# Performance work log

Hardware: AMD Instinct MI355X
Metric: run time of the kernel (lower is better)

Reference implementation:

```python
import jax, jax.numpy as jnp
import numpy as np

HEADS = 16

def setup_inputs() -> dict:
    key = jax.random.key(0)
    k1, k2, k3 = jax.random.split(key, 3)
    B, S, D = 2, 2048, 1024
    return {
        "query": jax.random.normal(k1, (B, S, D), dtype=jnp.float32),
        "key": jax.random.normal(k2, (B, S, D), dtype=jnp.float32),
        "value": jax.random.normal(k3, (B, S, D), dtype=jnp.float32),
    }

def reference(query, key, value):
    B, S, D = query.shape
    H = HEADS
    dh = D // H
    # split(-1) into H equal chunks == reshape to (B, S, H, dh)
    q = query.reshape(B, S, H, dh)
    k = key.reshape(B, S, H, dh)
    v = value.reshape(B, S, H, dh)
    scale = 1.0 / jnp.sqrt(jnp.asarray(dh, dtype=query.dtype))
    scores = jnp.einsum('bqhd,bkhd->bhqk', q, k) * scale  # [B,H,S,S]
    probs = jax.nn.softmax(scores, axis=-1)
    out = jnp.einsum('bhqk,bkhd->bqhd', probs, v)  # [B,S,H,dh]
    return out.reshape(B, S, D)
```

## Files before the change

### kernel.cpp

```cpp
#include <hip/hip_runtime.h>


#define B_ 2
#define S_ 2048
#define D_ 1024
#define H_ 16
#define DH 64
#define M_TILE 128
#define N_TILE 128
#define NITER (S_ / N_TILE)

typedef __bf16 bf16;
typedef __bf16 bf16x2 __attribute__((ext_vector_type(2)));
typedef __bf16 bf16x4 __attribute__((ext_vector_type(4)));
typedef __bf16 bf16x8 __attribute__((ext_vector_type(8)));
typedef float floatx4 __attribute__((ext_vector_type(4)));

#define K_STRIDE 68
#define V_STRIDE 132
#define K_BYTES (128 * K_STRIDE * 2)
#define V_BYTES (64 * V_STRIDE * 2)
#define O_STRIDE 36
#define O_BYTES (256 * O_STRIDE * 4)
#define ML_OFF  O_BYTES
#define SMEM_BYTES (ML_OFF + 512)

__device__ __forceinline__ float fast_exp2(float x) {
#if __has_builtin(__builtin_amdgcn_exp2f)
  return __builtin_amdgcn_exp2f(x);
#else
  return exp2f(x);
#endif
}

__device__ __forceinline__ bf16x8 cat8(bf16x4 a, bf16x4 b) {
  return __builtin_shufflevector(a, b, 0, 1, 2, 3, 4, 5, 6, 7);
}

__global__ __launch_bounds__(512, 4)
void attn_fwd(const float* __restrict__ Qg, const float* __restrict__ Kg,
              const float* __restrict__ Vg, float* __restrict__ Og) {
  __shared__ __align__(16) unsigned char smem[SMEM_BYTES];
  bf16*  Ksh = (bf16*)smem;
  bf16*  Vsh = (bf16*)(smem + K_BYTES);
  float* Osh = (float*)smem;
  float* Lsh = (float*)(smem + ML_OFF);

  const int tid  = threadIdx.x;
  const int lane = tid & 63;
  const int wave = tid >> 6;
  const int kw   = wave & 1;
  const int qw   = wave >> 1;
  const int col  = lane & 15;
  const int quad = lane >> 4;

  const int bid      = blockIdx.x;
  const int head_lin = bid & 31;
  const int qtile    = bid >> 5;
  const int b        = head_lin >> 4;
  const int h        = head_lin & 15;

  const float QSCALE = 0.125f * 1.44269504088896340736f;

  bf16x8 Qf[2][2];
#pragma unroll
  for (int qt = 0; qt < 2; ++qt) {
    const float* base = Qg + (size_t)(b * S_ + qtile * M_TILE + qw * 32 + qt * 16 + col) * D_
                        + h * DH + quad * 8;
#pragma unroll
    for (int ks = 0; ks < 2; ++ks) {
      float4 x0 = *(const float4*)(base + ks * 32);
      float4 x1 = *(const float4*)(base + ks * 32 + 4);
      bf16x8 f;
      f[0] = (bf16)(x0.x * QSCALE); f[1] = (bf16)(x0.y * QSCALE);
      f[2] = (bf16)(x0.z * QSCALE); f[3] = (bf16)(x0.w * QSCALE);
      f[4] = (bf16)(x1.x * QSCALE); f[5] = (bf16)(x1.y * QSCALE);
      f[6] = (bf16)(x1.z * QSCALE); f[7] = (bf16)(x1.w * QSCALE);
      Qf[qt][ks] = f;
    }
  }

  floatx4 accO[4][2];
  float l_lane[2] = {0.f, 0.f};
#pragma unroll
  for (int ft = 0; ft < 4; ++ft)
#pragma unroll
    for (int qt = 0; qt < 2; ++qt) accO[ft][qt] = (floatx4)0.f;

  const float* Kbase = Kg + (size_t)(b * S_) * D_ + h * DH;
  const float* Vbase = Vg + (size_t)(b * S_) * D_ + h * DH;

  const int krow0 = tid >> 4;
  const int kf4   = tid & 15;
  const int vk0   = (tid >> 3) * 2;
  const int vf0   = (tid & 7) * 8;

  for (int it = 0; it < NITER; ++it) {
    const int kb = it * N_TILE;

    float4 kx[4];
#pragma unroll
    for (int i = 0; i < 4; ++i)
      kx[i] = *(const float4*)(Kbase + (size_t)(kb + krow0 + 32 * i) * D_ + kf4 * 4);
    float4 va0 = *(const float4*)(Vbase + (size_t)(kb + vk0) * D_ + vf0);
    float4 va1 = *(const float4*)(Vbase + (size_t)(kb + vk0) * D_ + vf0 + 4);
    float4 vb0 = *(const float4*)(Vbase + (size_t)(kb + vk0 + 1) * D_ + vf0);
    float4 vb1 = *(const float4*)(Vbase + (size_t)(kb + vk0 + 1) * D_ + vf0 + 4);
#pragma unroll
    for (int i = 0; i < 4; ++i) {
      bf16x4 y = {(bf16)kx[i].x, (bf16)kx[i].y, (bf16)kx[i].z, (bf16)kx[i].w};
      *(bf16x4*)(Ksh + (krow0 + 32 * i) * K_STRIDE + kf4 * 4) = y;
    }
    {
      float a[8] = {va0.x, va0.y, va0.z, va0.w, va1.x, va1.y, va1.z, va1.w};
      float c[8] = {vb0.x, vb0.y, vb0.z, vb0.w, vb1.x, vb1.y, vb1.z, vb1.w};
#pragma unroll
      for (int j = 0; j < 8; ++j) {
        bf16x2 y = {(bf16)a[j], (bf16)c[j]};
        *(bf16x2*)(Vsh + (vf0 + j) * V_STRIDE + vk0) = y;
      }
    }
    __syncthreads();

    floatx4 accS[4][2];
#pragma unroll
    for (int kt = 0; kt < 4; ++kt) {
      const bf16* kp = Ksh + (kw * 64 + kt * 16 + col) * K_STRIDE + quad * 8;
      bf16x8 Ka0 = cat8(*(const bf16x4*)kp, *(const bf16x4*)(kp + 4));
      bf16x8 Ka1 = cat8(*(const bf16x4*)(kp + 32), *(const bf16x4*)(kp + 36));
#pragma unroll
      for (int qt = 0; qt < 2; ++qt) {
        floatx4 a = (floatx4)0.f;
        a = __builtin_amdgcn_mfma_f32_16x16x32_bf16(Ka0, Qf[qt][0], a, 0, 0, 0);
        a = __builtin_amdgcn_mfma_f32_16x16x32_bf16(Ka1, Qf[qt][1], a, 0, 0, 0);
        accS[kt][qt] = a;
      }
    }

#pragma unroll
    for (int qt = 0; qt < 2; ++qt) {
      float rs = 0.f;
#pragma unroll
      for (int kt = 0; kt < 4; ++kt)
#pragma unroll
        for (int r = 0; r < 4; ++r) {
          float p = fast_exp2(accS[kt][qt][r]);
          accS[kt][qt][r] = p;
          rs += p;
        }
      l_lane[qt] += rs;
    }

#pragma unroll
    for (int c = 0; c < 2; ++c) {
      bf16x8 Pf[2];
#pragma unroll
      for (int qt = 0; qt < 2; ++qt) {
        floatx4 p0 = accS[2 * c][qt], p1 = accS[2 * c + 1][qt];
        bf16x8 f = {(bf16)p0[0], (bf16)p0[1], (bf16)p0[2], (bf16)p0[3],
                    (bf16)p1[0], (bf16)p1[1], (bf16)p1[2], (bf16)p1[3]};
        Pf[qt] = f;
      }
#pragma unroll
      for (int ft = 0; ft < 4; ++ft) {
        const bf16* vp = Vsh + (ft * 16 + col) * V_STRIDE + kw * 64 + 32 * c + quad * 4;
        bf16x8 Va = cat8(*(const bf16x4*)vp, *(const bf16x4*)(vp + 16));
#pragma unroll
        for (int qt = 0; qt < 2; ++qt)
          accO[ft][qt] = __builtin_amdgcn_mfma_f32_16x16x32_bf16(Va, Pf[qt], accO[ft][qt], 0, 0, 0);
      }
    }
    __syncthreads();
  }

  float l_red[2];
#pragma unroll
  for (int qt = 0; qt < 2; ++qt) {
    float s = l_lane[qt];
    s += __shfl_xor(s, 16);
    s += __shfl_xor(s, 32);
    l_red[qt] = s;
  }

  if (kw == 1) {
    float* r = Osh + (qw * 64 + lane) * O_STRIDE;
#pragma unroll
    for (int qt = 0; qt < 2; ++qt)
#pragma unroll
      for (int ft = 0; ft < 4; ++ft)
        *(floatx4*)(r + (qt * 4 + ft) * 4) = accO[ft][qt];
    if (quad == 0) {
#pragma unroll
      for (int qt = 0; qt < 2; ++qt)
        Lsh[qw * 32 + qt * 16 + col] = l_red[qt];
    }
  }
  __syncthreads();

  if (kw == 0) {
    const float* r = Osh + (qw * 64 + lane) * O_STRIDE;
    float rl[2];
#pragma unroll
    for (int qt = 0; qt < 2; ++qt)
      rl[qt] = 1.0f / (l_red[qt] + Lsh[qw * 32 + qt * 16 + col]);
#pragma unroll
    for (int qt = 0; qt < 2; ++qt) {
      const int q = qtile * M_TILE + qw * 32 + qt * 16 + col;
      float* dst = Og + (size_t)(b * S_ + q) * D_ + h * DH + quad * 4;
#pragma unroll
      for (int ft = 0; ft < 4; ++ft) {
        floatx4 o = (accO[ft][qt] + *(const floatx4*)(r + (qt * 4 + ft) * 4)) * rl[qt];
        *(floatx4*)(dst + ft * 16) = o;
      }
    }
  }
}

extern "C" void kernel_launch(void* const* d_in, const int* in_sizes, int n_in,
                              void* d_out, int out_size, void* d_ws, size_t ws_size,
                              hipStream_t stream) {
  const float* Q = (const float*)d_in[0];
  const float* K = (const float*)d_in[1];
  const float* V = (const float*)d_in[2];
  float* O = (float*)d_out;
  dim3 grid(B_ * H_ * (S_ / M_TILE));
  dim3 block(512);
  hipLaunchKernelGGL(attn_fwd, grid, block, 0, stream, Q, K, V, O);
}
```

Measured before the change: 137.8 us.

## Pre-convert K/V to bf16 in workspace and double-buffer tiles via direct global-to-LDS loads

Adds a prep kernel that converts K to bf16 in a per-head layout and writes V transposed in bf16 into a workspace buffer. The attention kernel then streams tiles into a double-buffered, XOR-swizzled LDS with global_load_lds, prefetching the next tile while computing the current one. This removes the repeated fp32 K/V loads and in-kernel conversion that each of the 16 query tiles per head used to do, and drops one barrier per iteration. In exchange it adds an extra kernel launch, a workspace requirement and larger LDS use (64KB), which may lower occupancy. A fallback path keeps the old kernel for when no workspace is available.

```diff
diff --git a/kernel.cpp b/kernel.cpp
--- a/kernel.cpp
+++ b/kernel.cpp
@@ -1,4 +1,5 @@
 #include <hip/hip_runtime.h>
+#include <stdint.h>
 
 
 #define B_ 2
@@ -16,14 +17,16 @@
 typedef __bf16 bf16x8 __attribute__((ext_vector_type(8)));
 typedef float floatx4 __attribute__((ext_vector_type(4)));
 
-#define K_STRIDE 68
-#define V_STRIDE 132
-#define K_BYTES (128 * K_STRIDE * 2)
-#define V_BYTES (64 * V_STRIDE * 2)
+#define KB_HEAD (S_ * DH * 2)
+#define KB_TOTAL (B_ * H_ * KB_HEAD)
+#define VT_ROW (S_ * 2)
+#define WS_NEEDED (2u * KB_TOTAL)
+
+#define KTILE_B 16384
+#define BUF_B 32768
+#define LSH_OFF 65536
+#define SMEM_MAIN (LSH_OFF + 512)
 #define O_STRIDE 36
-#define O_BYTES (256 * O_STRIDE * 4)
-#define ML_OFF  O_BYTES
-#define SMEM_BYTES (ML_OFF + 512)
 
 __device__ __forceinline__ float fast_exp2(float x) {
 #if __has_builtin(__builtin_amdgcn_exp2f)
@@ -33,18 +36,70 @@
 #endif
 }
 
-__device__ __forceinline__ bf16x8 cat8(bf16x4 a, bf16x4 b) {
-  return __builtin_shufflevector(a, b, 0, 1, 2, 3, 4, 5, 6, 7);
+__device__ __forceinline__ void gl_lds16(const void* g, void* l) {
+  __builtin_amdgcn_global_load_lds(
+      (const __attribute__((address_space(1))) unsigned int*)g,
+      (__attribute__((address_space(3))) unsigned int*)l, 16, 0, 0);
+}
+
+__global__ __launch_bounds__(256)
+void prep(const float* __restrict__ Kg, const float* __restrict__ Vg,
+          unsigned char* __restrict__ ws) {
+  const int bid = blockIdx.x;
+  const int tid = threadIdx.x;
+  if (bid < 512) {
+    __shared__ __align__(16) bf16 VTsh[64][132];
+    const int head_lin = bid & 31, ktile = bid >> 5;
+    const int b = head_lin >> 4, h = head_lin & 15;
+    const int kb = ktile * 128;
+    const int vr0 = (tid >> 3) << 2;
+    const int vf0 = (tid & 7) << 3;
+    const float* Vbase = Vg + (size_t)(b * S_) * D_ + h * DH;
+    float vals[4][8];
+#pragma unroll
+    for (int rr = 0; rr < 4; ++rr) {
+      const float* vp = Vbase + (size_t)(kb + vr0 + rr) * D_ + vf0;
+      float4 a = *(const float4*)vp;
+      float4 c = *(const float4*)(vp + 4);
+      vals[rr][0] = a.x; vals[rr][1] = a.y; vals[rr][2] = a.z; vals[rr][3] = a.w;
+      vals[rr][4] = c.x; vals[rr][5] = c.y; vals[rr][6] = c.z; vals[rr][7] = c.w;
+    }
+    const int pbase = (vr0 & 96) + ((vr0 >> 2) & 3) * 8 + ((vr0 >> 4) & 1) * 4;
+#pragma unroll
+    for (int j = 0; j < 8; ++j) {
+      bf16x4 y = {(bf16)vals[0][j], (bf16)vals[1][j], (bf16)vals[2][j], (bf16)vals[3][j]};
+      *(bf16x4*)(&VTsh[vf0 + j][pbase]) = y;
+    }
+    __syncthreads();
+    const int f = tid >> 2, part = tid & 3;
+    unsigned char* dst = ws + KB_TOTAL + (size_t)(head_lin * 64 + f) * VT_ROW + kb * 2 + part * 64;
+#pragma unroll
+    for (int c16 = 0; c16 < 4; ++c16) {
+      bf16x8 v = *(const bf16x8*)(&VTsh[f][part * 32 + c16 * 8]);
+      *(bf16x8*)(dst + c16 * 16) = v;
+    }
+  } else {
+    const int cb = bid - 512;
+#pragma unroll
+    for (int i = 0; i < 8; ++i) {
+      int idx = cb * 2048 + i * 256 + tid;
+      int f4 = idx & 15;
+      int hh = (idx >> 4) & 15;
+      int s  = (idx >> 8) & 2047;
+      int bb = idx >> 19;
+      float4 x = *(const float4*)(Kg + (size_t)idx * 4);
+      bf16x4 y = {(bf16)x.x, (bf16)x.y, (bf16)x.z, (bf16)x.w};
+      *(bf16x4*)(ws + (size_t)(((bb * 16 + hh) * 2048 + s) * 16 + f4) * 8) = y;
+    }
+  }
 }
 
 __global__ __launch_bounds__(512, 4)
-void attn_fwd(const float* __restrict__ Qg, const float* __restrict__ Kg,
-              const float* __restrict__ Vg, float* __restrict__ Og) {
-  __shared__ __align__(16) unsigned char smem[SMEM_BYTES];
-  bf16*  Ksh = (bf16*)smem;
-  bf16*  Vsh = (bf16*)(smem + K_BYTES);
+void attn_fwd(const float* __restrict__ Qg, const unsigned char* __restrict__ Kb,
+              const unsigned char* __restrict__ VT, float* __restrict__ Og) {
+  __shared__ __align__(16) unsigned char smem[SMEM_MAIN];
   float* Osh = (float*)smem;
-  float* Lsh = (float*)(smem + ML_OFF);
+  float* Lsh = (float*)(smem + LSH_OFF);
 
   const int tid  = threadIdx.x;
   const int lane = tid & 63;
@@ -59,6 +114,9 @@
   const int qtile    = bid >> 5;
   const int b        = head_lin >> 4;
   const int h        = head_lin & 15;
+
+  const unsigned char* Khead = Kb + (size_t)head_lin * KB_HEAD;
+  const unsigned char* Vhead = VT + (size_t)head_lin * (DH * VT_ROW);
 
   const float QSCALE = 0.125f * 1.44269504088896340736f;
 
@@ -87,9 +145,193 @@
 #pragma unroll
     for (int qt = 0; qt < 2; ++qt) accO[ft][qt] = (floatx4)0.f;
 
+  const int krow_b = wave * 16 + (lane >> 3);
+  const int kcg    = lane & 7;
+  const int vf_b   = wave * 8 + (lane >> 4);
+  const int vcg    = lane & 15;
+
+  const int krow0   = kw * 64 + col;
+  const int ka0_off = krow0 * 128 + ((quad ^ (col & 7)) << 4);
+  const int ka1_off = krow0 * 128 + (((quad | 4) ^ (col & 7)) << 4);
+  const int va_c0   = KTILE_B + col * 256 + ((((kw << 3) | quad) ^ col) << 4);
+  const int va_c1   = KTILE_B + col * 256 + ((((kw << 3) | 4 | quad) ^ col) << 4);
+
+  auto dma_tile = [&](int kbk, int bufoff) {
+#pragma unroll
+    for (int t = 0; t < 2; ++t) {
+      const int r = krow_b + t * 8;
+      gl_lds16(Khead + (size_t)(kbk + r) * 128 + ((kcg ^ (r & 7)) << 4),
+               smem + bufoff + (wave * 16 + t * 8) * 128);
+    }
+#pragma unroll
+    for (int t = 0; t < 2; ++t) {
+      const int f = vf_b + t * 4;
+      gl_lds16(Vhead + (size_t)f * VT_ROW + kbk * 2 + ((vcg ^ (f & 15)) << 4),
+               smem + bufoff + KTILE_B + (wave * 8 + t * 4) * 256);
+    }
+  };
+
+  dma_tile(0, 0);
+  __syncthreads();
+
+  for (int it = 0; it < NITER; ++it) {
+    const int bc = (it & 1) << 15;
+    if (it + 1 < NITER) dma_tile((it + 1) * N_TILE, bc ^ BUF_B);
+
+    floatx4 accS[4][2];
+#pragma unroll
+    for (int kt = 0; kt < 4; ++kt) {
+      bf16x8 Ka0 = *(const bf16x8*)(smem + bc + ka0_off + kt * 2048);
+      bf16x8 Ka1 = *(const bf16x8*)(smem + bc + ka1_off + kt * 2048);
+#pragma unroll
+      for (int qt = 0; qt < 2; ++qt) {
+        floatx4 a = (floatx4)0.f;
+        a = __builtin_amdgcn_mfma_f32_16x16x32_bf16(Ka0, Qf[qt][0], a, 0, 0, 0);
+        a = __builtin_amdgcn_mfma_f32_16x16x32_bf16(Ka1, Qf[qt][1], a, 0, 0, 0);
+        accS[kt][qt] = a;
+      }
+    }
+
+#pragma unroll
+    for (int qt = 0; qt < 2; ++qt) {
+      float rs = 0.f;
+#pragma unroll
+      for (int kt = 0; kt < 4; ++kt)
+#pragma unroll
+        for (int r = 0; r < 4; ++r) {
+          float p = fast_exp2(accS[kt][qt][r]);
+          accS[kt][qt][r] = p;
+          rs += p;
+        }
+      l_lane[qt] += rs;
+    }
+
+#pragma unroll
+    for (int c = 0; c < 2; ++c) {
+      bf16x8 Pf[2];
+#pragma unroll
+      for (int qt = 0; qt < 2; ++qt) {
+        floatx4 p0 = accS[2 * c][qt], p1 = accS[2 * c + 1][qt];
+        bf16x8 f = {(bf16)p0[0], (bf16)p0[1], (bf16)p0[2], (bf16)p0[3],
+                    (bf16)p1[0], (bf16)p1[1], (bf16)p1[2], (bf16)p1[3]};
+        Pf[qt] = f;
+      }
+      const int vo = c ? va_c1 : va_c0;
+#pragma unroll
+      for (int ft = 0; ft < 4; ++ft) {
+        bf16x8 Va = *(const bf16x8*)(smem + bc + vo + ft * 4096);
+#pragma unroll
+        for (int qt = 0; qt < 2; ++qt)
+          accO[ft][qt] = __builtin_amdgcn_mfma_f32_16x16x32_bf16(Va, Pf[qt], accO[ft][qt], 0, 0, 0);
+      }
+    }
+    __syncthreads();
+  }
+
+  float l_red[2];
+#pragma unroll
+  for (int qt = 0; qt < 2; ++qt) {
+    float s = l_lane[qt];
+    s += __shfl_xor(s, 16);
+    s += __shfl_xor(s, 32);
+    l_red[qt] = s;
+  }
+
+  if (kw == 1) {
+    float* r = Osh + (qw * 64 + lane) * O_STRIDE;
+#pragma unroll
+    for (int qt = 0; qt < 2; ++qt)
+#pragma unroll
+      for (int ft = 0; ft < 4; ++ft)
+        *(floatx4*)(r + (qt * 4 + ft) * 4) = accO[ft][qt];
+    if (quad == 0) {
+#pragma unroll
+      for (int qt = 0; qt < 2; ++qt)
+        Lsh[qw * 32 + qt * 16 + col] = l_red[qt];
+    }
+  }
+  __syncthreads();
+
+  if (kw == 0) {
+    const float* r = Osh + (qw * 64 + lane) * O_STRIDE;
+    float rl[2];
+#pragma unroll
+    for (int qt = 0; qt < 2; ++qt)
+      rl[qt] = 1.0f / (l_red[qt] + Lsh[qw * 32 + qt * 16 + col]);
+#pragma unroll
+    for (int qt = 0; qt < 2; ++qt) {
+      const int q = qtile * M_TILE + qw * 32 + qt * 16 + col;
+      float* dst = Og + (size_t)(b * S_ + q) * D_ + h * DH + quad * 4;
+#pragma unroll
+      for (int ft = 0; ft < 4; ++ft) {
+        floatx4 o = (accO[ft][qt] + *(const floatx4*)(r + (qt * 4 + ft) * 4)) * rl[qt];
+        *(floatx4*)(dst + ft * 16) = o;
+      }
+    }
+  }
+}
+
+#define FB_K_STRIDE 68
+#define FB_V_STRIDE 132
+#define FB_K_BYTES (128 * FB_K_STRIDE * 2)
+#define FB_V_BYTES (64 * FB_V_STRIDE * 2)
+#define FB_ML_OFF (FB_K_BYTES + FB_V_BYTES)
+#define FB_SMEM (FB_ML_OFF + 2048)
+
+__device__ __forceinline__ bf16x8 cat8(bf16x4 a, bf16x4 b) {
+  return __builtin_shufflevector(a, b, 0, 1, 2, 3, 4, 5, 6, 7);
+}
+
+__global__ __launch_bounds__(512, 4)
+void attn_fwd_fb(const float* __restrict__ Qg, const float* __restrict__ Kg,
+                 const float* __restrict__ Vg, float* __restrict__ Og) {
+  __shared__ __align__(16) unsigned char smem[FB_SMEM > (256 * O_STRIDE * 4 + 2048) ? FB_SMEM : (256 * O_STRIDE * 4 + 2048)];
+  bf16*  Ksh = (bf16*)smem;
+  bf16*  Vsh = (bf16*)(smem + FB_K_BYTES);
+  float* Osh = (float*)smem;
+  float* Lsh = (float*)(smem + 256 * O_STRIDE * 4);
+
+  const int tid  = threadIdx.x;
+  const int lane = tid & 63;
+  const int wave = tid >> 6;
+  const int kw   = wave & 1;
+  const int qw   = wave >> 1;
+  const int col  = lane & 15;
+  const int quad = lane >> 4;
+  const int bid      = blockIdx.x;
+  const int head_lin = bid & 31;
+  const int qtile    = bid >> 5;
+  const int b        = head_lin >> 4;
+  const int h        = head_lin & 15;
+  const float QSCALE = 0.125f * 1.44269504088896340736f;
+
+  bf16x8 Qf[2][2];
+#pragma unroll
+  for (int qt = 0; qt < 2; ++qt) {
+    const float* base = Qg + (size_t)(b * S_ + qtile * M_TILE + qw * 32 + qt * 16 + col) * D_
+                        + h * DH + quad * 8;
+#pragma unroll
+    for (int ks = 0; ks < 2; ++ks) {
+      float4 x0 = *(const float4*)(base + ks * 32);
+      float4 x1 = *(const float4*)(base + ks * 32 + 4);
+      bf16x8 f;
+      f[0] = (bf16)(x0.x * QSCALE); f[1] = (bf16)(x0.y * QSCALE);
+      f[2] = (bf16)(x0.z * QSCALE); f[3] = (bf16)(x0.w * QSCALE);
+      f[4] = (bf16)(x1.x * QSCALE); f[5] = (bf16)(x1.y * QSCALE);
+      f[6] = (bf16)(x1.z * QSCALE); f[7] = (bf16)(x1.w * QSCALE);
+      Qf[qt][ks] = f;
+    }
+  }
+
+  floatx4 accO[4][2];
+  float l_lane[2] = {0.f, 0.f};
+#pragma unroll
+  for (int ft = 0; ft < 4; ++ft)
+#pragma unroll
+    for (int qt = 0; qt < 2; ++qt) accO[ft][qt] = (floatx4)0.f;
+
   const float* Kbase = Kg + (size_t)(b * S_) * D_ + h * DH;
   const float* Vbase = Vg + (size_t)(b * S_) * D_ + h * DH;
-
   const int krow0 = tid >> 4;
   const int kf4   = tid & 15;
   const int vk0   = (tid >> 3) * 2;
@@ -97,7 +339,6 @@
 
   for (int it = 0; it < NITER; ++it) {
     const int kb = it * N_TILE;
-
     float4 kx[4];
 #pragma unroll
     for (int i = 0; i < 4; ++i)
@@ -109,7 +350,7 @@
 #pragma unroll
     for (int i = 0; i < 4; ++i) {
       bf16x4 y = {(bf16)kx[i].x, (bf16)kx[i].y, (bf16)kx[i].z, (bf16)kx[i].w};
-      *(bf16x4*)(Ksh + (krow0 + 32 * i) * K_STRIDE + kf4 * 4) = y;
+      *(bf16x4*)(Ksh + (krow0 + 32 * i) * FB_K_STRIDE + kf4 * 4) = y;
     }
     {
       float a[8] = {va0.x, va0.y, va0.z, va0.w, va1.x, va1.y, va1.z, va1.w};
@@ -117,7 +358,7 @@
 #pragma unroll
       for (int j = 0; j < 8; ++j) {
         bf16x2 y = {(bf16)a[j], (bf16)c[j]};
-        *(bf16x2*)(Vsh + (vf0 + j) * V_STRIDE + vk0) = y;
+        *(bf16x2*)(Vsh + (vf0 + j) * FB_V_STRIDE + vk0) = y;
       }
     }
     __syncthreads();
@@ -125,7 +366,7 @@
     floatx4 accS[4][2];
 #pragma unroll
     for (int kt = 0; kt < 4; ++kt) {
-      const bf16* kp = Ksh + (kw * 64 + kt * 16 + col) * K_STRIDE + quad * 8;
+      const bf16* kp = Ksh + (kw * 64 + kt * 16 + col) * FB_K_STRIDE + quad * 8;
       bf16x8 Ka0 = cat8(*(const bf16x4*)kp, *(const bf16x4*)(kp + 4));
       bf16x8 Ka1 = cat8(*(const bf16x4*)(kp + 32), *(const bf16x4*)(kp + 36));
 #pragma unroll
@@ -136,7 +377,6 @@
         accS[kt][qt] = a;
       }
     }
-
 #pragma unroll
     for (int qt = 0; qt < 2; ++qt) {
       float rs = 0.f;
@@ -150,7 +390,6 @@
         }
       l_lane[qt] += rs;
     }
-
 #pragma unroll
     for (int c = 0; c < 2; ++c) {
       bf16x8 Pf[2];
@@ -163,7 +402,7 @@
       }
 #pragma unroll
       for (int ft = 0; ft < 4; ++ft) {
-        const bf16* vp = Vsh + (ft * 16 + col) * V_STRIDE + kw * 64 + 32 * c + quad * 4;
+        const bf16* vp = Vsh + (ft * 16 + col) * FB_V_STRIDE + kw * 64 + 32 * c + quad * 4;
         bf16x8 Va = cat8(*(const bf16x4*)vp, *(const bf16x4*)(vp + 16));
 #pragma unroll
         for (int qt = 0; qt < 2; ++qt)
@@ -181,7 +420,6 @@
     s += __shfl_xor(s, 32);
     l_red[qt] = s;
   }
-
   if (kw == 1) {
     float* r = Osh + (qw * 64 + lane) * O_STRIDE;
 #pragma unroll
@@ -196,7 +434,6 @@
     }
   }
   __syncthreads();
-
   if (kw == 0) {
     const float* r = Osh + (qw * 64 + lane) * O_STRIDE;
     float rl[2];
@@ -223,7 +460,13 @@
   const float* K = (const float*)d_in[1];
   const float* V = (const float*)d_in[2];
   float* O = (float*)d_out;
-  dim3 grid(B_ * H_ * (S_ / M_TILE));
-  dim3 block(512);
-  hipLaunchKernelGGL(attn_fwd, grid, block, 0, stream, Q, K, V, O);
-}
+  if (ws_size >= WS_NEEDED && d_ws != nullptr) {
+    unsigned char* ws = (unsigned char*)d_ws;
+    hipLaunchKernelGGL(prep, dim3(1024), dim3(256), 0, stream, K, V, ws);
+    hipLaunchKernelGGL(attn_fwd, dim3(B_ * H_ * (S_ / M_TILE)), dim3(512), 0, stream,
+                       Q, ws, ws + KB_TOTAL, O);
+  } else {
+    hipLaunchKernelGGL(attn_fwd_fb, dim3(B_ * H_ * (S_ / M_TILE)), dim3(512), 0, stream,
+                       Q, K, V, O);
+  }
+}
```

After: 129.9 us. 5.7% less time.
